# Kernel tuning notes

Hardware: AMD Instinct MI355X
Metric: run time of the kernel (lower is better)

Reference implementation:

```python
import jax, jax.numpy as jnp
import numpy as np

B, T, D = 2, 2048, 2048
H = 8
KEY_DIM, VAL_DIM = 1024, 2048   # expand_k=0.5, expand_v=1.0
HK, HV = KEY_DIM // H, VAL_DIM // H
LOW_RANK = 16
GATE_NORM = 16.0
CHUNK = 64
HIDDEN = (D * 4 * 2 // 3 + 63) // 64 * 64  # 5504, exactly as GLUFFN.__init__
EPS = 1e-6


def rmsnorm(x, w):
    return x * jax.lax.rsqrt(jnp.mean(x * x, axis=-1, keepdims=True) + EPS) * w


def setup_inputs() -> dict:
    key = jax.random.key(0)
    ks = jax.random.split(key, 12)
    w = lambda k, s: jax.random.normal(k, s, jnp.float32) * 0.02
    return {
        "x": jax.random.normal(ks[0], (B, T, D), jnp.float32),
        "norm1_w": jnp.ones((D,), jnp.float32),
        "wq": w(ks[1], (D, KEY_DIM)),
        "wk": w(ks[2], (D, KEY_DIM)),
        "wv": w(ks[3], (D, VAL_DIM)),
        "gk_w1": w(ks[4], (D, LOW_RANK)),
        "gk_w2": w(ks[5], (LOW_RANK, KEY_DIM)),
        "gk_b": jnp.zeros((KEY_DIM,), jnp.float32),
        "wg": w(ks[6], (D, VAL_DIM)),
        "gnorm_w": jnp.ones((HV,), jnp.float32),
        "wo": w(ks[7], (VAL_DIM, D)),
        "ffn_norm_w": jnp.ones((D,), jnp.float32),
        "w_gate": w(ks[8], (D, HIDDEN)),
        "w_up": w(ks[9], (D, HIDDEN)),
        "w_down": w(ks[10], (HIDDEN, D)),
    }


def _gla(h, wq, wk, wv, gk_w1, gk_w2, gk_b, wg, gnorm_w, wo):
    # Gated linear attention, chunk-parallel form (fla-style):
    #   S_t = diag(exp(g_t)) S_{t-1} + k_t^T v_t ;  o_t = q_t S_t
    Bb, Tt, _ = h.shape
    nc = Tt // CHUNK

    def split(t, hd):  # [B,T,H*hd] -> [nc,B,H,CHUNK,hd]
        t = t.reshape(Bb, nc, CHUNK, H, hd)
        return jnp.transpose(t, (1, 0, 3, 2, 4))

    q = split(h @ wq, HK) * (HK ** -0.5)
    k = split(h @ wk, HK)
    v = split(h @ wv, HV)
    # low-rank forget gate, log-sigmoid scaled by gate_logit_normalizer=16
    g = split(jax.nn.log_sigmoid(h @ gk_w1 @ gk_w2 + gk_b) / GATE_NORM, HK)

    mask = jnp.tril(jnp.ones((CHUNK, CHUNK), jnp.float32))

    def step(S, inp):
        qc, kc, vc, gc = inp                       # [B,H,C,*]
        b = jnp.cumsum(gc, axis=-2)                # cumulative log-decay within chunk
        qe = qc * jnp.exp(b)
        A = jnp.einsum('bhik,bhjk->bhij', qe, kc * jnp.exp(-b)) * mask
        o = jnp.einsum('bhck,bhkv->bhcv', qe, S) + jnp.einsum('bhij,bhjv->bhiv', A, vc)
        bl = b[:, :, -1:, :]                       # decay to end of chunk
        S = jnp.exp(bl[:, :, 0, :])[..., None] * S + \
            jnp.einsum('bhck,bhcv->bhkv', kc * jnp.exp(bl - b), vc)
        return S, o

    S0 = jnp.zeros((Bb, H, HK, HV), h.dtype)
    _, o = jax.lax.scan(step, S0, (q, k, v, g))    # o: [nc,B,H,C,HV]
    o = jnp.transpose(o, (1, 0, 3, 2, 4)).reshape(Bb, Tt, H, HV)

    gate = (h @ wg).reshape(Bb, Tt, H, HV)
    # per-head RMSNorm + swish output gate (FusedRMSNormSwishGate)
    o = rmsnorm(o, gnorm_w) * gate * jax.nn.sigmoid(gate)
    return o.reshape(Bb, Tt, VAL_DIM) @ wo


def reference(x, norm1_w, wq, wk, wv, gk_w1, gk_w2, gk_b, wg, gnorm_w, wo,
              ffn_norm_w, w_gate, w_up, w_down):
    h = rmsnorm(x, norm1_w)
    x = x + _gla(h, wq, wk, wv, gk_w1, gk_w2, gk_b, wg, gnorm_w, wo)
    h2 = rmsnorm(x, ffn_norm_w)
    ffn = (jax.nn.silu(h2 @ w_gate) * (h2 @ w_up)) @ w_down  # GLUFFN, dropout=eval
    return x + ffn
```

## Files before the change

kernel.cpp:

```cpp
#include <hip/hip_runtime.h>

typedef unsigned short u16;
typedef __attribute__((ext_vector_type(8))) short bh8;
typedef __attribute__((ext_vector_type(4))) float f4;

__device__ __forceinline__ float bf2f(u16 u) {
  union { unsigned int i; float f; } x; x.i = ((unsigned int)u) << 16; return x.f;
}
__device__ __forceinline__ u16 f2bf(float f) {
  union { float f; unsigned int i; } x; x.f = f;
  unsigned int r = x.i + 0x7fffu + ((x.i >> 16) & 1u);
  return (u16)(r >> 16);
}
__device__ __forceinline__ f4 mfma16(bh8 a, bh8 b, f4 c) {
  return __builtin_amdgcn_mfma_f32_16x16x32_bf16(a, b, c, 0, 0, 0);
}
__device__ __forceinline__ void gload16(const void* g, void* l) {
  __builtin_amdgcn_global_load_lds(
      (const __attribute__((address_space(1))) void*)g,
      (__attribute__((address_space(3))) void*)l, 16, 0, 0);
}

__device__ __forceinline__ bh8 rd8(const u16* arr, int row, int col, int rowbytes) {
  return *(const bh8*)((const char*)arr + row * rowbytes + ((col * 2) ^ ((row & 7) << 4)));
}

__global__ __launch_bounds__(256)
void wtrans_k(const float* __restrict__ src, u16* __restrict__ dst, int R, int C,
              int rmul, int roff) {
  __shared__ float tile[32][33];
  int tx = threadIdx.x & 31, ty = threadIdx.x >> 5;
  int c0 = blockIdx.x * 32, r0 = blockIdx.y * 32;
#pragma unroll
  for (int yy = 0; yy < 32; yy += 8)
    tile[ty + yy][tx] = src[(size_t)(r0 + ty + yy) * C + c0 + tx];
  __syncthreads();
#pragma unroll
  for (int yy = 0; yy < 32; yy += 8)
    dst[(size_t)((c0 + ty + yy) * rmul + roff) * R + r0 + tx] = f2bf(tile[tx][ty + yy]);
}

__global__ __launch_bounds__(256)
void rmsnorm_k(const float* __restrict__ x, const float* __restrict__ w,
               u16* __restrict__ out) {
  int row = blockIdx.x, t = threadIdx.x;
  const float* xr = x + (size_t)row * 2048;
  float4 a = ((const float4*)xr)[t * 2];
  float4 b = ((const float4*)xr)[t * 2 + 1];
  float ss = a.x*a.x + a.y*a.y + a.z*a.z + a.w*a.w
           + b.x*b.x + b.y*b.y + b.z*b.z + b.w*b.w;
#pragma unroll
  for (int s = 32; s > 0; s >>= 1) ss += __shfl_xor(ss, s, 64);
  __shared__ float red[4];
  if ((t & 63) == 0) red[t >> 6] = ss;
  __syncthreads();
  float rr = rsqrtf((red[0] + red[1] + red[2] + red[3]) * (1.0f / 2048.0f) + 1e-6f);
  float v[8] = {a.x, a.y, a.z, a.w, b.x, b.y, b.z, b.w};
  int c0 = t * 8;
  u16* orow = out + (size_t)row * 2048 + c0;
#pragma unroll
  for (int j = 0; j < 8; ++j) orow[j] = f2bf(v[j] * rr * w[c0 + j]);
}

template <int EPI, int BN, typename OutT>
__global__ __launch_bounds__(512, 2)
void gemm2(const u16* __restrict__ A, const u16* __restrict__ Bt,
           OutT* __restrict__ C, void* __restrict__ aux, float scale,
           int M, int N, int K, int gx) {
  constexpr int MB = (BN == 256) ? 8 : 4;
  constexpr int NBS = (BN == 256) ? 2 : 1;
  constexpr int SB = 16384 + BN * 64;
  __shared__ char lds[3 * SB];
  int t = threadIdx.x, lane = t & 63, w = t >> 6;
  int c_ = lane & 15, r_ = lane >> 4;
  int wm = (BN == 256) ? (w >> 2) : (w >> 1);
  int wn = (BN == 256) ? (w & 3) : (w & 1);

  int nwg = gridDim.x;
  int wg = (blockIdx.x & 7) * (nwg >> 3) + (blockIdx.x >> 3);
  int gy = nwg / gx;
  int bx = wg / gy, by = wg % gy;
  int m0 = by * 256, n0 = bx * BN;

  const char* baseA[2];
#pragma unroll
  for (int h = 0; h < 2; ++h) {
    int p = h * 512 + t;
    int cc = p ^ ((p >> 3) & 7);
    baseA[h] = (const char*)A + ((size_t)(m0 + (cc >> 2)) * K + (cc & 3) * 8) * 2;
  }
  const char* baseB[NBS];
#pragma unroll
  for (int h = 0; h < NBS; ++h) {
    int p = h * 512 + t;
    int cc = p ^ ((p >> 3) & 7);
    baseB[h] = (const char*)Bt + ((size_t)(n0 + (cc >> 2)) * K + (cc & 3) * 8) * 2;
  }
  int offA[MB], offB[4];
#pragma unroll
  for (int mb = 0; mb < MB; ++mb) {
    int cc = (wm * (MB * 16) + mb * 16 + c_) * 4 + r_;
    offA[mb] = (cc ^ ((cc >> 3) & 7)) * 16;
  }
#pragma unroll
  for (int nb = 0; nb < 4; ++nb) {
    int cc = (wn * 64 + nb * 16 + c_) * 4 + r_;
    offB[nb] = (cc ^ ((cc >> 3) & 7)) * 16 + 16384;
  }
  int ldsW = w * 1024;

  f4 z4 = {0.f, 0.f, 0.f, 0.f};
  f4 acc[MB][4];
#pragma unroll
  for (int mb = 0; mb < MB; ++mb)
#pragma unroll
    for (int nb = 0; nb < 4; ++nb) acc[mb][nb] = z4;

  int NT = K >> 5;

#define STAGEA(S, ko)                                                       \
  {                                                                         \
    _Pragma("unroll") for (int h = 0; h < 2; ++h)                           \
        gload16(baseA[h] + (ko), lds + (S) * SB + h * 8192 + ldsW);         \
  }
#define STAGEB(S, ko)                                                       \
  {                                                                         \
    _Pragma("unroll") for (int h = 0; h < NBS; ++h)                         \
        gload16(baseB[h] + (ko), lds + (S) * SB + 16384 + h * 8192 + ldsW); \
  }
#define WAIT_VM()                                                           \
  if (BN == 256) { asm volatile("s_waitcnt vmcnt(4)" ::: "memory"); }       \
  else { asm volatile("s_waitcnt vmcnt(3)" ::: "memory"); }
#define KTILE(S)                                                            \
  {                                                                         \
    int kts = kt + 2; if (kts >= NT) kts -= NT;                             \
    constexpr int S2 = ((S) + 2) % 3;                                       \
    bh8 fb[4], fa[4];                                                       \
    _Pragma("unroll") for (int nb = 0; nb < 4; ++nb)                        \
        fb[nb] = *(const bh8*)(lds + (S) * SB + offB[nb]);                  \
    _Pragma("unroll") for (int mb = 0; mb < 4; ++mb)                        \
        fa[mb] = *(const bh8*)(lds + (S) * SB + offA[mb]);                  \
    STAGEA(S2, kts << 6);                                                   \
    asm volatile("s_waitcnt lgkmcnt(0)" ::: "memory");                      \
    __builtin_amdgcn_sched_barrier(0);                                      \
    if (BN == 256) {                                                        \
      bh8 fa2[4];                                                           \
      _Pragma("unroll") for (int mb = 0; mb < 4; ++mb)                      \
          fa2[mb] = *(const bh8*)(lds + (S) * SB + offA[(MB / 2) + mb]);    \
      STAGEB(S2, kts << 6);                                                 \
      __builtin_amdgcn_sched_barrier(0);                                    \
      __builtin_amdgcn_s_setprio(1);                                        \
      _Pragma("unroll") for (int mb = 0; mb < 4; ++mb)                      \
          _Pragma("unroll") for (int nb = 0; nb < 4; ++nb)                  \
              acc[mb][nb] = mfma16(fa[mb], fb[nb], acc[mb][nb]);            \
      __builtin_amdgcn_s_setprio(0);                                        \
      asm volatile("s_waitcnt lgkmcnt(0)" ::: "memory");                    \
      __builtin_amdgcn_sched_barrier(0);                                    \
      __builtin_amdgcn_s_setprio(1);                                        \
      _Pragma("unroll") for (int mb = 0; mb < 4; ++mb)                      \
          _Pragma("unroll") for (int nb = 0; nb < 4; ++nb)                  \
              acc[(MB / 2) + mb][nb] =                                      \
                  mfma16(fa2[mb], fb[nb], acc[(MB / 2) + mb][nb]);          \
      __builtin_amdgcn_s_setprio(0);                                        \
      __builtin_amdgcn_sched_barrier(0);                                    \
    } else {                                                                \
      STAGEB(S2, kts << 6);                                                 \
      __builtin_amdgcn_sched_barrier(0);                                    \
      __builtin_amdgcn_s_setprio(1);                                        \
      _Pragma("unroll") for (int mb = 0; mb < 4; ++mb)                      \
          _Pragma("unroll") for (int nb = 0; nb < 4; ++nb)                  \
              acc[mb][nb] = mfma16(fa[mb], fb[nb], acc[mb][nb]);            \
      __builtin_amdgcn_s_setprio(0);                                        \
      __builtin_amdgcn_sched_barrier(0);                                    \
    }                                                                       \
    WAIT_VM();                                                              \
    __builtin_amdgcn_s_barrier();                                           \
    asm volatile("" ::: "memory");                                          \
  }

  STAGEA(0, 0); STAGEB(0, 0);
  STAGEA(1, 64); STAGEB(1, 64);
  WAIT_VM();
  __builtin_amdgcn_s_barrier();
  asm volatile("" ::: "memory");

  int kt = 0;
  while (true) {
    KTILE(0); if (++kt == NT) break;
    KTILE(1); if (++kt == NT) break;
    KTILE(2); if (++kt == NT) break;
  }
  asm volatile("s_waitcnt vmcnt(0)" ::: "memory");
#undef KTILE
#undef WAIT_VM
#undef STAGEA
#undef STAGEB

  int rowBase = m0 + wm * (MB * 16);
#pragma unroll
  for (int mb = 0; mb < MB; ++mb) {
#pragma unroll
    for (int rr = 0; rr < 4; ++rr) {
      int row = rowBase + mb * 16 + r_ * 4 + rr;
#pragma unroll
      for (int nb = 0; nb < 4; ++nb) {
        int col = n0 + wn * 64 + nb * 16 + c_;
        float val = acc[mb][nb][rr];
        if (EPI == 1) {
          ((float*)C)[(size_t)row * N + col] = val + ((const float*)aux)[(size_t)row * N + col];
        } else if (EPI == 5) {
          if (col < 1024) ((u16*)C)[(size_t)row * 1024 + col] = f2bf(val * scale);
          else ((u16*)aux)[(size_t)row * 1024 + col - 1024] = f2bf(val);
        } else if (EPI == 4) {
          if (col < 2048) {
            int bb = row >> 11, t2 = row & 2047;
            int pan = ((bb << 5) + (t2 >> 6)) * 8 + (col >> 8);
            int ii = t2 & 63, vv = col & 255;
            *(u16*)((char*)C + (size_t)pan * 32768 + vv * 128 + ((ii * 2) ^ ((vv & 7) << 4)))
                = f2bf(val);
          } else {
            ((u16*)aux)[(size_t)row * 2048 + col - 2048] = f2bf(val);
          }
        } else if (EPI == 6) {
          float other = __shfl_xor(val, 1, 64);
          if (lane & 1) {
            float gv = other;
            ((u16*)C)[(size_t)row * 5504 + (col >> 1)] = f2bf(val * (gv / (1.f + expf(-gv))));
          }
        }
      }
    }
  }
}

__global__ __launch_bounds__(256)
void lowrank_k(const u16* __restrict__ h, const float* __restrict__ w1,
               const float* __restrict__ w2, const float* __restrict__ bias,
               float* __restrict__ g) {
  int row = blockIdx.x, t = threadIdx.x, lane = t & 63, wave = t >> 6;
  const u16* hr = h + (size_t)row * 2048;
  bh8 hv = *(const bh8*)&hr[t * 8];
  float p[16];
#pragma unroll
  for (int j = 0; j < 16; ++j) p[j] = 0.f;
#pragma unroll
  for (int kk = 0; kk < 8; ++kk) {
    float f = bf2f((u16)hv[kk]);
    const float* wrow = w1 + (size_t)(t * 8 + kk) * 16;
#pragma unroll
    for (int j = 0; j < 16; ++j) p[j] += f * wrow[j];
  }
#pragma unroll
  for (int j = 0; j < 16; ++j)
#pragma unroll
    for (int s = 32; s > 0; s >>= 1) p[j] += __shfl_xor(p[j], s, 64);
  __shared__ float gl[4][16];
  if (lane == 0) {
#pragma unroll
    for (int j = 0; j < 16; ++j) gl[wave][j] = p[j];
  }
  __syncthreads();
  float glow[16];
#pragma unroll
  for (int j = 0; j < 16; ++j) glow[j] = gl[0][j] + gl[1][j] + gl[2][j] + gl[3][j];
  float* grow = g + (size_t)row * 1024;
#pragma unroll
  for (int nn = 0; nn < 4; ++nn) {
    int n = nn * 256 + t;
    float z = bias[n];
#pragma unroll
    for (int j = 0; j < 16; ++j) z += glow[j] * w2[j * 1024 + n];
    float ls = fminf(z, 0.f) - log1pf(expf(-fabsf(z)));
    grow[n] = ls * (1.0f / 16.0f);
  }
}

__global__ __launch_bounds__(128)
void gprep_k(u16* __restrict__ q, u16* __restrict__ k, const float* __restrict__ g,
             u16* __restrict__ keT, float* __restrict__ ebl) {
  int bid = blockIdx.x;
  int h = bid & 7, bc = bid >> 3;
  int b = bc >> 5, c = bc & 31;
  int ch = threadIdx.x;
  size_t base = ((size_t)(b * 2048 + c * 64)) * 1024 + h * 128 + ch;
  char* keTp = (char*)keT + (size_t)bid * 16384 + ch * 128;
  int sw = (ch & 7) << 4;
  float bacc = 0.f;
  for (int i8 = 0; i8 < 8; ++i8) {
    u16 kp[8];
#pragma unroll
    for (int e = 0; e < 8; ++e) {
      size_t off = base + (size_t)(i8 * 8 + e) * 1024;
      bacc += g[off];
      float eb = __expf(bacc);
      float reb = __builtin_amdgcn_rcpf(eb);
      float qv = bf2f(q[off]), kv = bf2f(k[off]);
      q[off] = f2bf(qv * eb);
      u16 kev = f2bf(kv * reb);
      k[off] = kev;
      kp[e] = kev;
    }
    *(bh8*)(keTp + ((i8 * 16) ^ sw)) = *(const bh8*)kp;
  }
  ebl[(size_t)bid * 128 + ch] = __expf(bacc);
}

__global__ __launch_bounds__(256)
void gla_scan(const u16* __restrict__ qg, const u16* __restrict__ kg,
              const u16* __restrict__ keTg, const u16* __restrict__ vTg,
              const float* __restrict__ eblg, float* __restrict__ outp) {
  __shared__ u16 qeL[64 * 128];
  __shared__ u16 keL[64 * 128];
  __shared__ u16 kTL[128 * 64];
  __shared__ u16 vTL[64 * 64];
  __shared__ u16 AL[64 * 64];
  __shared__ u16 SbL[64 * 128];
  __shared__ float SfL[64][133];

  int t = threadIdx.x, lane = t & 63, w = t >> 6;
  int vb = blockIdx.x & 3, bh = blockIdx.x >> 2;
  int b = bh >> 3, h = bh & 7;
  int c_ = lane & 15, r_ = lane >> 4;
  f4 z4 = {0.f, 0.f, 0.f, 0.f};

  for (int i = t; i < 64 * 128; i += 256) SbL[i] = 0;
  for (int i = t; i < 64 * 133; i += 256) ((float*)SfL)[i] = 0.f;

  const char* qbase = (const char*)qg + (size_t)b * 2048 * 2048 + h * 256;
  const char* kbase = (const char*)kg + (size_t)b * 2048 * 2048 + h * 256;
  int rowoff = (t >> 4) * 2048 + (t & 15) * 16;
  int4 pq[4], pk[4], pkt[4], pvt[2];

#define LOADCH(cc)                                                              \
  {                                                                             \
    const char* qc = qbase + (size_t)(cc) * 64 * 2048;                          \
    const char* kc = kbase + (size_t)(cc) * 64 * 2048;                          \
    int panel_ = ((b * 32 + (cc)) * 8 + h);                                     \
    const char* ktc = (const char*)keTg + (size_t)panel_ * 16384;               \
    const char* vtc = (const char*)vTg + (size_t)panel_ * 32768 + vb * 8192;    \
    _Pragma("unroll")                                                           \
    for (int j = 0; j < 4; ++j) {                                               \
      pq[j] = *(const int4*)(qc + j * 16 * 2048 + rowoff);                      \
      pk[j] = *(const int4*)(kc + j * 16 * 2048 + rowoff);                      \
      pkt[j] = *(const int4*)(ktc + j * 4096 + t * 16);                         \
    }                                                                           \
    _Pragma("unroll")                                                           \
    for (int j = 0; j < 2; ++j) pvt[j] = *(const int4*)(vtc + j * 4096 + t * 16); \
  }

  LOADCH(0);
  for (int c = 0; c < 32; ++c) {
#pragma unroll
    for (int j = 0; j < 4; ++j) {
      int L = j * 4096 + t * 16;
      int d = (L & ~255) | ((L & 255) ^ (((L >> 8) & 7) << 4));
      *(int4*)((char*)qeL + d) = pq[j];
      *(int4*)((char*)keL + d) = pk[j];
      *(int4*)((char*)kTL + L) = pkt[j];
    }
#pragma unroll
    for (int j = 0; j < 2; ++j) *(int4*)((char*)vTL + j * 4096 + t * 16) = pvt[j];
    if (c < 31) LOADCH(c + 1);
    int panel = ((b * 32 + c) * 8 + h);
    float eblr[2][4];
#pragma unroll
    for (int kt = 0; kt < 2; ++kt)
#pragma unroll
      for (int r = 0; r < 4; ++r)
        eblr[kt][r] = eblg[(size_t)panel * 128 + w * 32 + kt * 16 + r_ * 4 + r];
    __syncthreads();

    f4 accA[4] = {z4, z4, z4, z4};
    f4 accS[2][4] = {{z4, z4, z4, z4}, {z4, z4, z4, z4}};
#pragma unroll
    for (int ks = 0; ks < 4; ++ks) {
      bh8 a = rd8(qeL, w * 16 + c_, ks * 32 + r_ * 8, 256);
#pragma unroll
      for (int n = 0; n < 4; ++n)
        accA[n] = mfma16(a, rd8(keL, n * 16 + c_, ks * 32 + r_ * 8, 256), accA[n]);
    }
#pragma unroll
    for (int ks = 0; ks < 2; ++ks) {
      bh8 bf_[4];
#pragma unroll
      for (int n = 0; n < 4; ++n) bf_[n] = rd8(vTL, n * 16 + c_, ks * 32 + r_ * 8, 128);
#pragma unroll
      for (int kt = 0; kt < 2; ++kt) {
        bh8 a = rd8(kTL, w * 32 + kt * 16 + c_, ks * 32 + r_ * 8, 128);
#pragma unroll
        for (int n = 0; n < 4; ++n) accS[kt][n] = mfma16(a, bf_[n], accS[kt][n]);
      }
    }
#pragma unroll
    for (int n = 0; n < 4; ++n)
#pragma unroll
      for (int r = 0; r < 4; ++r) {
        int i = w * 16 + r_ * 4 + r, j = n * 16 + c_;
        *(u16*)((char*)AL + i * 128 + ((j * 2) ^ ((i & 7) << 4))) =
            (j <= i) ? f2bf(accA[n][r]) : (u16)0;
      }
    __syncthreads();

    f4 acco[4] = {z4, z4, z4, z4};
#pragma unroll
    for (int ks = 0; ks < 4; ++ks) {
      bh8 a = rd8(qeL, w * 16 + c_, ks * 32 + r_ * 8, 256);
#pragma unroll
      for (int n = 0; n < 4; ++n)
        acco[n] = mfma16(a, rd8(SbL, n * 16 + c_, ks * 32 + r_ * 8, 256), acco[n]);
    }
#pragma unroll
    for (int ks = 0; ks < 2; ++ks) {
      bh8 a = rd8(AL, w * 16 + c_, ks * 32 + r_ * 8, 128);
#pragma unroll
      for (int n = 0; n < 4; ++n)
        acco[n] = mfma16(a, rd8(vTL, n * 16 + c_, ks * 32 + r_ * 8, 128), acco[n]);
    }
    {
      size_t obase = (size_t)(b * 2048 + c * 64 + w * 16 + r_ * 4) * 2048 + h * 256 + vb * 64;
#pragma unroll
      for (int n = 0; n < 4; ++n)
#pragma unroll
        for (int r = 0; r < 4; ++r)
          outp[obase + (size_t)r * 2048 + n * 16 + c_] = acco[n][r];
    }
    __syncthreads();

#pragma unroll
    for (int kt = 0; kt < 2; ++kt)
#pragma unroll
      for (int n = 0; n < 4; ++n)
#pragma unroll
        for (int r = 0; r < 4; ++r) {
          int kk = w * 32 + kt * 16 + r_ * 4 + r;
          int vcol = n * 16 + c_;
          float nv = eblr[kt][r] * (SfL[vcol][kk] + accS[kt][n][r]);
          SfL[vcol][kk] = nv;
          *(u16*)((char*)SbL + vcol * 256 + ((kk * 2) ^ ((vcol & 7) << 4))) = f2bf(nv);
        }
    __syncthreads();
  }
#undef LOADCH
}

__global__ __launch_bounds__(256)
void ogate_k(const float* __restrict__ o, const u16* __restrict__ gate,
             const float* __restrict__ gw, u16* __restrict__ og) {
  int tok = blockIdx.x, t = threadIdx.x;
  int head = t >> 5, l32 = t & 31, v0 = l32 * 8;
  size_t base = (size_t)tok * 2048 + head * 256 + v0;
  float4 a = *(const float4*)&o[base];
  float4 b = *(const float4*)&o[base + 4];
  float ov[8] = {a.x, a.y, a.z, a.w, b.x, b.y, b.z, b.w};
  float ss = 0.f;
#pragma unroll
  for (int j = 0; j < 8; ++j) ss += ov[j] * ov[j];
#pragma unroll
  for (int s = 16; s > 0; s >>= 1) ss += __shfl_xor(ss, s, 32);
  float rr = rsqrtf(ss * (1.0f / 256.0f) + 1e-6f);
#pragma unroll
  for (int j = 0; j < 8; ++j) {
    float gv = bf2f(gate[base + j]);
    float val = ov[j] * rr * gw[v0 + j];
    og[base + j] = f2bf(val * gv / (1.f + expf(-gv)));
  }
}

extern "C" void kernel_launch(void* const* d_in, const int* in_sizes, int n_in,
                              void* d_out, int out_size, void* d_ws, size_t ws_size,
                              hipStream_t stream) {
  (void)in_sizes; (void)n_in; (void)out_size; (void)ws_size;
  const float* x = (const float*)d_in[0];
  const float* n1w = (const float*)d_in[1];
  const float* wq = (const float*)d_in[2];
  const float* wk = (const float*)d_in[3];
  const float* wv = (const float*)d_in[4];
  const float* gw1 = (const float*)d_in[5];
  const float* gw2 = (const float*)d_in[6];
  const float* gb = (const float*)d_in[7];
  const float* wg = (const float*)d_in[8];
  const float* gnw = (const float*)d_in[9];
  const float* wo = (const float*)d_in[10];
  const float* fnw = (const float*)d_in[11];
  const float* wgate = (const float*)d_in[12];
  const float* wup = (const float*)d_in[13];
  const float* wdown = (const float*)d_in[14];
  float* out = (float*)d_out;

  char* ws = (char*)d_ws;
  size_t off = 0;
  auto alloc = [&](size_t bytes) { size_t p = off; off += (bytes + 255) & ~(size_t)255; return p; };
  u16* wqT = (u16*)(ws + alloc(2ull * 1024 * 2048));
  u16* wkT = (u16*)(ws + alloc(2ull * 1024 * 2048));
  u16* wvT = (u16*)(ws + alloc(2ull * 2048 * 2048));
  u16* wgT = (u16*)(ws + alloc(2ull * 2048 * 2048));
  u16* woT = (u16*)(ws + alloc(2ull * 2048 * 2048));
  u16* btGU = (u16*)(ws + alloc(2ull * 11008 * 2048));
  u16* wdT = (u16*)(ws + alloc(2ull * 2048 * 5504));
  u16* h_bf = (u16*)(ws + alloc(2ull * 4096 * 2048));
  u16* q_bf = (u16*)(ws + alloc(2ull * 4096 * 1024));
  u16* k_bf = (u16*)(ws + alloc(2ull * 4096 * 1024));
  u16* vT_g = (u16*)(ws + alloc(2ull * 4096 * 2048));
  u16* gate_bf = (u16*)(ws + alloc(2ull * 4096 * 2048));
  float* g_f = (float*)(ws + alloc(4ull * 4096 * 1024));
  float* o_f = (float*)(ws + alloc(4ull * 4096 * 2048));
  u16* mid = (u16*)(ws + alloc(2ull * 4096 * 5504));
  float* ebl_g = (float*)(ws + alloc(4ull * 512 * 128));
  u16* keT_g = h_bf;
  u16* og = h_bf;
  u16* h2 = q_bf;
  float* x2 = o_f;

  dim3 blk(256);
  dim3 blk2(512);
  wtrans_k<<<dim3(32, 64), blk, 0, stream>>>(wq, wqT, 2048, 1024, 1, 0);
  wtrans_k<<<dim3(32, 64), blk, 0, stream>>>(wk, wkT, 2048, 1024, 1, 0);
  wtrans_k<<<dim3(64, 64), blk, 0, stream>>>(wv, wvT, 2048, 2048, 1, 0);
  wtrans_k<<<dim3(64, 64), blk, 0, stream>>>(wg, wgT, 2048, 2048, 1, 0);
  wtrans_k<<<dim3(64, 64), blk, 0, stream>>>(wo, woT, 2048, 2048, 1, 0);
  wtrans_k<<<dim3(172, 64), blk, 0, stream>>>(wgate, btGU, 2048, 5504, 2, 0);
  wtrans_k<<<dim3(172, 64), blk, 0, stream>>>(wup, btGU, 2048, 5504, 2, 1);
  wtrans_k<<<dim3(64, 172), blk, 0, stream>>>(wdown, wdT, 5504, 2048, 1, 0);

  rmsnorm_k<<<4096, blk, 0, stream>>>(x, n1w, h_bf);

  gemm2<5, 128, u16><<<256, blk2, 0, stream>>>(h_bf, wqT, q_bf, k_bf, 0.08838834764831845f,
                                               4096, 2048, 2048, 16);
  gemm2<4, 256, u16><<<256, blk2, 0, stream>>>(h_bf, wvT, vT_g, gate_bf, 1.f,
                                               4096, 4096, 2048, 16);
  lowrank_k<<<4096, blk, 0, stream>>>(h_bf, gw1, gw2, gb, g_f);

  gprep_k<<<512, dim3(128), 0, stream>>>(q_bf, k_bf, g_f, keT_g, ebl_g);

  gla_scan<<<64, blk, 0, stream>>>(q_bf, k_bf, keT_g, vT_g, ebl_g, o_f);

  ogate_k<<<4096, blk, 0, stream>>>(o_f, gate_bf, gnw, og);

  gemm2<1, 128, float><<<256, blk2, 0, stream>>>(og, woT, x2, (void*)x, 1.f,
                                                 4096, 2048, 2048, 16);

  rmsnorm_k<<<4096, blk, 0, stream>>>(x2, fnw, h2);

  gemm2<6, 256, u16><<<688, blk2, 0, stream>>>(h2, btGU, mid, nullptr, 1.f,
                                               4096, 11008, 2048, 43);
  gemm2<1, 128, float><<<256, blk2, 0, stream>>>(mid, wdT, out, x2, 1.f,
                                                 4096, 2048, 5504, 16);
}
```

Measured before the change: 955.8 us.

## Switch GEMM mainloop to 64-wide K tiles with double buffering

The GEMM now stages 64-wide K tiles instead of 32-wide ones, using two LDS buffers in place of three. Each tile runs two MFMA sub-steps, and a new row-major swizzled LDS layout replaces the old one. This halves the barriers and loop iterations per K and issues larger batched global-to-LDS loads. In exchange, it waits with vmcnt(0) every tile instead of keeping two tiles in flight, which may expose load latency. LDS use also grows, which could lower occupancy at BN=256.

```diff
diff --git a/kernel.cpp b/kernel.cpp
--- a/kernel.cpp
+++ b/kernel.cpp
@@ -68,9 +68,9 @@
            OutT* __restrict__ C, void* __restrict__ aux, float scale,
            int M, int N, int K, int gx) {
   constexpr int MB = (BN == 256) ? 8 : 4;
-  constexpr int NBS = (BN == 256) ? 2 : 1;
-  constexpr int SB = 16384 + BN * 64;
-  __shared__ char lds[3 * SB];
+  constexpr int NBL = BN / 64;
+  constexpr int SB = (256 + BN) * 128;
+  __shared__ char lds[2 * SB];
   int t = threadIdx.x, lane = t & 63, w = t >> 6;
   int c_ = lane & 15, r_ = lane >> 4;
   int wm = (BN == 256) ? (w >> 2) : (w >> 1);
@@ -82,30 +82,31 @@
   int bx = wg / gy, by = wg % gy;
   int m0 = by * 256, n0 = bx * BN;
 
-  const char* baseA[2];
-#pragma unroll
-  for (int h = 0; h < 2; ++h) {
-    int p = h * 512 + t;
-    int cc = p ^ ((p >> 3) & 7);
-    baseA[h] = (const char*)A + ((size_t)(m0 + (cc >> 2)) * K + (cc & 3) * 8) * 2;
-  }
-  const char* baseB[NBS];
-#pragma unroll
-  for (int h = 0; h < NBS; ++h) {
-    int p = h * 512 + t;
-    int cc = p ^ ((p >> 3) & 7);
-    baseB[h] = (const char*)Bt + ((size_t)(n0 + (cc >> 2)) * K + (cc & 3) * 8) * 2;
-  }
-  int offA[MB], offB[4];
+  int trow = t >> 3;
+  int kchunk = (t & 7) ^ (trow & 7);
+  const char* baseA[4];
+#pragma unroll
+  for (int l = 0; l < 4; ++l)
+    baseA[l] = (const char*)A + ((size_t)(m0 + l * 64 + trow) * K + kchunk * 8) * 2;
+  const char* baseB[NBL];
+#pragma unroll
+  for (int l = 0; l < NBL; ++l)
+    baseB[l] = (const char*)Bt + ((size_t)(n0 + l * 64 + trow) * K + kchunk * 8) * 2;
+
+  int offA[MB][2], offB[4][2];
 #pragma unroll
   for (int mb = 0; mb < MB; ++mb) {
-    int cc = (wm * (MB * 16) + mb * 16 + c_) * 4 + r_;
-    offA[mb] = (cc ^ ((cc >> 3) & 7)) * 16;
+    int row = wm * (MB * 16) + mb * 16 + c_;
+#pragma unroll
+    for (int ks = 0; ks < 2; ++ks)
+      offA[mb][ks] = row * 128 + (((ks * 4 + r_) ^ (row & 7)) << 4);
   }
 #pragma unroll
   for (int nb = 0; nb < 4; ++nb) {
-    int cc = (wn * 64 + nb * 16 + c_) * 4 + r_;
-    offB[nb] = (cc ^ ((cc >> 3) & 7)) * 16 + 16384;
+    int n = wn * 64 + nb * 16 + c_;
+#pragma unroll
+    for (int ks = 0; ks < 2; ++ks)
+      offB[nb][ks] = 32768 + n * 128 + (((ks * 4 + r_) ^ (n & 7)) << 4);
   }
   int ldsW = w * 1024;
 
@@ -116,85 +117,65 @@
 #pragma unroll
     for (int nb = 0; nb < 4; ++nb) acc[mb][nb] = z4;
 
-  int NT = K >> 5;
-
-#define STAGEA(S, ko)                                                       \
+  int NT = K >> 6;
+
+#define STAGE(S, ko)                                                        \
   {                                                                         \
-    _Pragma("unroll") for (int h = 0; h < 2; ++h)                           \
-        gload16(baseA[h] + (ko), lds + (S) * SB + h * 8192 + ldsW);         \
-  }
-#define STAGEB(S, ko)                                                       \
+    _Pragma("unroll") for (int l = 0; l < 4; ++l)                           \
+        gload16(baseA[l] + (ko), lds + (S) * SB + l * 8192 + ldsW);         \
+    _Pragma("unroll") for (int l = 0; l < NBL; ++l)                         \
+        gload16(baseB[l] + (ko), lds + (S) * SB + 32768 + l * 8192 + ldsW); \
+  }
+#define KT64(S)                                                             \
   {                                                                         \
-    _Pragma("unroll") for (int h = 0; h < NBS; ++h)                         \
-        gload16(baseB[h] + (ko), lds + (S) * SB + 16384 + h * 8192 + ldsW); \
-  }
-#define WAIT_VM()                                                           \
-  if (BN == 256) { asm volatile("s_waitcnt vmcnt(4)" ::: "memory"); }       \
-  else { asm volatile("s_waitcnt vmcnt(3)" ::: "memory"); }
-#define KTILE(S)                                                            \
-  {                                                                         \
-    int kts = kt + 2; if (kts >= NT) kts -= NT;                             \
-    constexpr int S2 = ((S) + 2) % 3;                                       \
-    bh8 fb[4], fa[4];                                                       \
-    _Pragma("unroll") for (int nb = 0; nb < 4; ++nb)                        \
-        fb[nb] = *(const bh8*)(lds + (S) * SB + offB[nb]);                  \
-    _Pragma("unroll") for (int mb = 0; mb < 4; ++mb)                        \
-        fa[mb] = *(const bh8*)(lds + (S) * SB + offA[mb]);                  \
-    STAGEA(S2, kts << 6);                                                   \
-    asm volatile("s_waitcnt lgkmcnt(0)" ::: "memory");                      \
-    __builtin_amdgcn_sched_barrier(0);                                      \
-    if (BN == 256) {                                                        \
-      bh8 fa2[4];                                                           \
+    int kts = kt + 1; if (kts >= NT) kts -= NT;                             \
+    STAGE((S) ^ 1, kts << 7);                                               \
+    _Pragma("unroll")                                                       \
+    for (int ks = 0; ks < 2; ++ks) {                                        \
+      bh8 fb[4], fa[4];                                                     \
+      _Pragma("unroll") for (int nb = 0; nb < 4; ++nb)                      \
+          fb[nb] = *(const bh8*)(lds + (S) * SB + offB[nb][ks]);            \
       _Pragma("unroll") for (int mb = 0; mb < 4; ++mb)                      \
-          fa2[mb] = *(const bh8*)(lds + (S) * SB + offA[(MB / 2) + mb]);    \
-      STAGEB(S2, kts << 6);                                                 \
-      __builtin_amdgcn_sched_barrier(0);                                    \
-      __builtin_amdgcn_s_setprio(1);                                        \
-      _Pragma("unroll") for (int mb = 0; mb < 4; ++mb)                      \
-          _Pragma("unroll") for (int nb = 0; nb < 4; ++nb)                  \
-              acc[mb][nb] = mfma16(fa[mb], fb[nb], acc[mb][nb]);            \
-      __builtin_amdgcn_s_setprio(0);                                        \
+          fa[mb] = *(const bh8*)(lds + (S) * SB + offA[mb][ks]);            \
       asm volatile("s_waitcnt lgkmcnt(0)" ::: "memory");                    \
       __builtin_amdgcn_sched_barrier(0);                                    \
-      __builtin_amdgcn_s_setprio(1);                                        \
-      _Pragma("unroll") for (int mb = 0; mb < 4; ++mb)                      \
-          _Pragma("unroll") for (int nb = 0; nb < 4; ++nb)                  \
-              acc[(MB / 2) + mb][nb] =                                      \
-                  mfma16(fa2[mb], fb[nb], acc[(MB / 2) + mb][nb]);          \
-      __builtin_amdgcn_s_setprio(0);                                        \
-      __builtin_amdgcn_sched_barrier(0);                                    \
-    } else {                                                                \
-      STAGEB(S2, kts << 6);                                                 \
-      __builtin_amdgcn_sched_barrier(0);                                    \
-      __builtin_amdgcn_s_setprio(1);                                        \
+      __builtin_amdgcn_s_setprio(1);                                       \
       _Pragma("unroll") for (int mb = 0; mb < 4; ++mb)                      \
           _Pragma("unroll") for (int nb = 0; nb < 4; ++nb)                  \
               acc[mb][nb] = mfma16(fa[mb], fb[nb], acc[mb][nb]);            \
       __builtin_amdgcn_s_setprio(0);                                        \
       __builtin_amdgcn_sched_barrier(0);                                    \
+      if constexpr (MB == 8) {                                              \
+        bh8 fa2[4];                                                         \
+        _Pragma("unroll") for (int mb = 0; mb < 4; ++mb)                    \
+            fa2[mb] = *(const bh8*)(lds + (S) * SB + offA[4 + mb][ks]);     \
+        asm volatile("s_waitcnt lgkmcnt(0)" ::: "memory");                  \
+        __builtin_amdgcn_sched_barrier(0);                                  \
+        __builtin_amdgcn_s_setprio(1);                                     \
+        _Pragma("unroll") for (int mb = 0; mb < 4; ++mb)                    \
+            _Pragma("unroll") for (int nb = 0; nb < 4; ++nb)                \
+                acc[4 + mb][nb] = mfma16(fa2[mb], fb[nb], acc[4 + mb][nb]); \
+        __builtin_amdgcn_s_setprio(0);                                      \
+        __builtin_amdgcn_sched_barrier(0);                                  \
+      }                                                                     \
     }                                                                       \
-    WAIT_VM();                                                              \
+    asm volatile("s_waitcnt vmcnt(0)" ::: "memory");                        \
     __builtin_amdgcn_s_barrier();                                           \
     asm volatile("" ::: "memory");                                          \
   }
 
-  STAGEA(0, 0); STAGEB(0, 0);
-  STAGEA(1, 64); STAGEB(1, 64);
-  WAIT_VM();
+  STAGE(0, 0);
+  asm volatile("s_waitcnt vmcnt(0)" ::: "memory");
   __builtin_amdgcn_s_barrier();
   asm volatile("" ::: "memory");
 
   int kt = 0;
   while (true) {
-    KTILE(0); if (++kt == NT) break;
-    KTILE(1); if (++kt == NT) break;
-    KTILE(2); if (++kt == NT) break;
-  }
-  asm volatile("s_waitcnt vmcnt(0)" ::: "memory");
-#undef KTILE
-#undef WAIT_VM
-#undef STAGEA
-#undef STAGEB
+    KT64(0); if (++kt == NT) break;
+    KT64(1); if (++kt == NT) break;
+  }
+#undef KT64
+#undef STAGE
 
   int rowBase = m0 + wm * (MB * 16);
 #pragma unroll
```

Result: slower. 1.897 ms (+98.5%).
